# Performance work log

Measured on AMD Instinct MI355X. Metric: run time of the kernel, lower is better.

Reference implementation:

```python
import jax, jax.numpy as jnp
import numpy as np

B, H, W, C, NH = 4, 64, 64, 512, 16
HD = C // NH
BIAS_LEVEL = 0.1
LN_EPS = 1e-5


def layernorm(x, g, b):
    m = jnp.mean(x, axis=-1, keepdims=True)
    v = jnp.mean(jnp.square(x - m), axis=-1, keepdims=True)
    return (x - m) * jax.lax.rsqrt(v + LN_EPS) * g + b


def partition(x, idx):
    # x: [B, L, C] -> windows [nW, S, C]
    xg = x.reshape(B, H, W, C)
    if idx == 0:  # horizontal strips: window = one row of length W
        return xg.reshape(B * H, W, C)
    else:  # vertical strips: window = one column of length H, ordered by column
        return xg.transpose(0, 2, 1, 3).reshape(B * W, H, C)


def unpartition(w, idx):
    # w: [nW, S, C] -> [B, L, C]
    if idx == 0:
        return w.reshape(B, H * W, C)
    else:
        return w.reshape(B, W, H, C).transpose(0, 2, 1, 3).reshape(B, H * W, C)


def eg_attention(q, k, v, res_x, rpe, idx):
    # q,k,v: [B, L, C]; res_x: [B, L, C]; rpe: [1, NH, S, S]
    S = rpe.shape[-1]
    nW = (B * H * W) // S

    def to_heads(t):
        return partition(t, idx).reshape(nW, S, NH, HD).transpose(0, 2, 1, 3)

    qh, kh, vh = to_heads(q), to_heads(k), to_heads(v)  # [nW, NH, S, HD]
    attn = jnp.einsum('whsd,whtd->whst', qh, kh) + BIAS_LEVEL * rpe
    # gating mask from raw scores
    M = jnp.mean(jnp.abs(attn), axis=(1, 2, 3), keepdims=True)  # [nW,1,1,1]
    M = M / jnp.max(M)
    M = jnp.maximum(M, 0.5)
    # L2-normalize rows, trig transform
    norm = jnp.sqrt(jnp.sum(jnp.square(attn), axis=-1, keepdims=True))
    attn = attn / jnp.maximum(norm, 1e-12)
    attn = 1.0 - jnp.cos(attn * (jnp.pi / 2))
    attn = attn * M
    out = jnp.einsum('whst,whtd->whsd', attn, vh)  # [nW, NH, S, HD]
    out = out.transpose(0, 2, 1, 3).reshape(nW, S, C)
    out = unpartition(out, idx)  # [B, L, C]
    # masked residual: res_x is chunked sequentially (row-major), as in the source
    res = res_x.reshape(nW, S, C) * (1.0 - M[:, 0])
    res = res.reshape(B, H * W, C)
    return out + res


def eg_block(x, rpe, idx, ln1_g, ln1_b, wqkv, wproj, bproj, ln2_g, ln2_b,
             wfc1, bfc1, wfc2, bfc2):
    img = layernorm(x, ln1_g, ln1_b)
    qkv = img @ wqkv  # [B, L, 3C]
    q, k, v = jnp.split(qkv, 3, axis=-1)
    att = eg_attention(q, k, v, x, rpe, idx)
    att = att @ wproj + bproj
    x = x + att
    h = layernorm(x, ln2_g, ln2_b)
    h = jax.nn.gelu(h @ wfc1 + bfc1, approximate=False) @ wfc2 + bfc2
    return x + h


def setup_inputs() -> dict:
    key = jax.random.key(0)
    ks = jax.random.split(key, 16)
    d = {
        'x': jax.random.normal(ks[0], (B, H * W, C), jnp.float32),
        'rpe0': jax.random.normal(ks[1], (1, NH, W, W), jnp.float32),
        'rpe1': jax.random.normal(ks[2], (1, NH, H, H), jnp.float32),
    }
    for i, blk in enumerate(['0', '1']):
        kk = jax.random.split(ks[3 + i], 8)
        d['ln1_g' + blk] = jnp.ones((C,), jnp.float32)
        d['ln1_b' + blk] = jnp.zeros((C,), jnp.float32)
        d['wqkv' + blk] = jax.random.normal(kk[0], (C, 3 * C), jnp.float32) * 0.02
        d['wproj' + blk] = jax.random.normal(kk[1], (C, C), jnp.float32) * 0.02
        d['bproj' + blk] = jnp.zeros((C,), jnp.float32)
        d['ln2_g' + blk] = jnp.ones((C,), jnp.float32)
        d['ln2_b' + blk] = jnp.zeros((C,), jnp.float32)
        d['wfc1_' + blk] = jax.random.normal(kk[2], (C, 4 * C), jnp.float32) * 0.02
        d['bfc1_' + blk] = jnp.zeros((4 * C,), jnp.float32)
        d['wfc2_' + blk] = jax.random.normal(kk[3], (4 * C, C), jnp.float32) * 0.02
        d['bfc2_' + blk] = jnp.zeros((C,), jnp.float32)
    return d


def reference(x, rpe0, rpe1,
              ln1_g0, ln1_b0, wqkv0, wproj0, bproj0, ln2_g0, ln2_b0,
              wfc1_0, bfc1_0, wfc2_0, bfc2_0,
              ln1_g1, ln1_b1, wqkv1, wproj1, bproj1, ln2_g1, ln2_b1,
              wfc1_1, bfc1_1, wfc2_1, bfc2_1):
    x = eg_block(x, rpe0, 0, ln1_g0, ln1_b0, wqkv0, wproj0, bproj0,
                 ln2_g0, ln2_b0, wfc1_0, bfc1_0, wfc2_0, bfc2_0)
    x = eg_block(x, rpe1, 1, ln1_g1, ln1_b1, wqkv1, wproj1, bproj1,
                 ln2_g1, ln2_b1, wfc1_1, bfc1_1, wfc2_1, bfc2_1)
    return x
```

## Files before the change

kernel.cpp:

```cpp
#include <hip/hip_runtime.h>
#include <cstdint>
#include <cstddef>

typedef __bf16 bf16;
typedef __attribute__((ext_vector_type(4))) float f32x4;
typedef __attribute__((ext_vector_type(8))) __bf16 bf16x8;
typedef __attribute__((ext_vector_type(4))) __bf16 bf16x4;

static __device__ __forceinline__ f32x4 mfma16(bf16x8 a, bf16x8 b, f32x4 c) {
    return __builtin_amdgcn_mfma_f32_16x16x32_bf16(a, b, c, 0, 0, 0);
}

#define GLOAD_LDS16(gsrc, ldst)                                              \
    __builtin_amdgcn_global_load_lds(                                        \
        (const __attribute__((address_space(1))) void*)(gsrc),               \
        (__attribute__((address_space(3))) void*)(ldst), 16, 0, 0)

__global__ __launch_bounds__(256)
void transpose_cast(const float* __restrict__ W, bf16* __restrict__ Wt, int K, int N) {
    __shared__ float tile[32][33];
    const int n0 = blockIdx.x * 32, k0 = blockIdx.y * 32;
    const int tx = threadIdx.x & 31, ty = threadIdx.x >> 5;
    #pragma unroll
    for (int i = ty; i < 32; i += 8)
        tile[i][tx] = W[(size_t)(k0 + i) * N + n0 + tx];
    __syncthreads();
    #pragma unroll
    for (int i = ty; i < 32; i += 8)
        Wt[(size_t)(n0 + i) * K + k0 + tx] = (bf16)tile[tx][i];
}

__global__ __launch_bounds__(256)
void ln_kernel(const float* __restrict__ x, const float* __restrict__ g,
               const float* __restrict__ b, bf16* __restrict__ out) {
    const int row = blockIdx.x * 4 + (threadIdx.x >> 6);
    const int lane = threadIdx.x & 63;
    const float* p = x + (size_t)row * 512 + lane * 8;
    const float4 a0 = *(const float4*)p;
    const float4 a1 = *(const float4*)(p + 4);
    float vx[8] = {a0.x, a0.y, a0.z, a0.w, a1.x, a1.y, a1.z, a1.w};
    float s = 0.f, ss = 0.f;
    #pragma unroll
    for (int k = 0; k < 8; ++k) { s += vx[k]; ss += vx[k] * vx[k]; }
    #pragma unroll
    for (int m = 1; m < 64; m <<= 1) {
        s  += __shfl_xor(s, m);
        ss += __shfl_xor(ss, m);
    }
    const float mean = s * (1.0f / 512.0f);
    const float var  = ss * (1.0f / 512.0f) - mean * mean;
    const float inv  = rsqrtf(var + 1e-5f);
    const int c0 = lane * 8;
    const float4 g0 = *(const float4*)&g[c0], g1 = *(const float4*)&g[c0 + 4];
    const float4 b0 = *(const float4*)&b[c0], b1 = *(const float4*)&b[c0 + 4];
    const float gv[8] = {g0.x, g0.y, g0.z, g0.w, g1.x, g1.y, g1.z, g1.w};
    const float bv[8] = {b0.x, b0.y, b0.z, b0.w, b1.x, b1.y, b1.z, b1.w};
    bf16x8 o;
    #pragma unroll
    for (int k = 0; k < 8; ++k)
        o[k] = (bf16)((vx[k] - mean) * inv * gv[k] + bv[k]);
    *(bf16x8*)&out[(size_t)row * 512 + c0] = o;
}

template <int EPI>
__global__ __launch_bounds__(256)
void gemm_bt(const bf16* __restrict__ A, const bf16* __restrict__ Bt,
             int N, int K, const float* __restrict__ bias,
             const float* __restrict__ res, float* __restrict__ outf,
             bf16* __restrict__ outh) {
    __shared__ __align__(16) bf16 lsA[128 * 32];
    __shared__ __align__(16) bf16 lsB[128 * 32];
    const int bn = blockIdx.x, bm = blockIdx.y;
    const int tid = threadIdx.x, lane = tid & 63, wv = tid >> 6;
    const int wm = (wv & 1) * 64, wn = (wv >> 1) * 64;
    const int l15 = lane & 15, lg = lane >> 4;
    f32x4 acc[4][4] = {};
    const size_t abase = (size_t)bm * 128 * K;
    const size_t bbase = (size_t)bn * 128 * K;
    const int srow = (lane >> 2);
    const int sseg = (lane & 3) * 8;
    for (int kt = 0; kt < K; kt += 32) {
        __syncthreads();
        #pragma unroll
        for (int c = 0; c < 2; ++c) {
            const int chunk = wv * 2 + c;
            const int row = chunk * 16 + srow;
            GLOAD_LDS16(&A[abase + (size_t)row * K + kt + sseg], &lsA[chunk * 512]);
            GLOAD_LDS16(&Bt[bbase + (size_t)row * K + kt + sseg], &lsB[chunk * 512]);
        }
        __syncthreads();
        bf16x8 af[4], bfr[4];
        #pragma unroll
        for (int i = 0; i < 4; ++i)
            af[i] = *(const bf16x8*)&lsA[(wm + i * 16 + l15) * 32 + lg * 8];
        #pragma unroll
        for (int j = 0; j < 4; ++j)
            bfr[j] = *(const bf16x8*)&lsB[(wn + j * 16 + l15) * 32 + lg * 8];
        #pragma unroll
        for (int i = 0; i < 4; ++i)
            #pragma unroll
            for (int j = 0; j < 4; ++j)
                acc[i][j] = mfma16(af[i], bfr[j], acc[i][j]);
    }
    #pragma unroll
    for (int i = 0; i < 4; ++i) {
        #pragma unroll
        for (int r = 0; r < 4; ++r) {
            const size_t row = (size_t)bm * 128 + wm + i * 16 + lg * 4 + r;
            #pragma unroll
            for (int j = 0; j < 4; ++j) {
                const int col = bn * 128 + wn + j * 16 + l15;
                const float v = acc[i][j][r];
                if constexpr (EPI == 0) {
                    outh[row * N + col] = (bf16)v;
                } else if constexpr (EPI == 1) {
                    outf[row * N + col] = v + bias[col] + res[row * N + col];
                } else {
                    const float t = v + bias[col];
                    const float gl = 0.5f * t * (1.0f + erff(t * 0.70710678118f));
                    outh[row * N + col] = (bf16)gl;
                }
            }
        }
    }
}

__global__ __launch_bounds__(256)
void attn_stats(const bf16* __restrict__ qkv, const float* __restrict__ rpe,
                float* __restrict__ Mraw4, int idx) {
    __shared__ float lsum[4];
    const int bid = blockIdx.x;
    const int w = bid >> 2;
    const int tid = threadIdx.x, lane = tid & 63, wv = tid >> 6;
    const int h = (bid & 3) * 4 + wv;
    const int l15 = lane & 15, lg = lane >> 4;
    const long gbase = (idx == 0) ? (long)w * 64 : ((long)(w >> 6) * 4096 + (w & 63));
    const long gstride = (idx == 0) ? 1 : 64;
    bf16x8 kf[4];
    #pragma unroll
    for (int i = 0; i < 4; ++i) {
        const long gs = gbase + (long)(i * 16 + l15) * gstride;
        kf[i] = *(const bf16x8*)&qkv[gs * 1536 + 512 + h * 32 + lg * 8];
    }
    const float* rh = rpe + h * 4096;
    float asum = 0.f;
    #pragma unroll
    for (int mi = 0; mi < 4; ++mi) {
        const long gs = gbase + (long)(mi * 16 + l15) * gstride;
        const bf16x8 qf = *(const bf16x8*)&qkv[gs * 1536 + h * 32 + lg * 8];
        f32x4 sc[4] = {};
        #pragma unroll
        for (int ni = 0; ni < 4; ++ni) sc[ni] = mfma16(qf, kf[ni], sc[ni]);
        #pragma unroll
        for (int r = 0; r < 4; ++r) {
            const int srow = mi * 16 + lg * 4 + r;
            #pragma unroll
            for (int ni = 0; ni < 4; ++ni)
                asum += fabsf(sc[ni][r] + 0.1f * rh[srow * 64 + ni * 16 + l15]);
        }
    }
    #pragma unroll
    for (int m = 1; m < 64; m <<= 1) asum += __shfl_xor(asum, m);
    if (lane == 0) lsum[wv] = asum;
    __syncthreads();
    if (tid == 0) Mraw4[bid] = lsum[0] + lsum[1] + lsum[2] + lsum[3];
}

__global__ __launch_bounds__(256)
void mcalc(const float* __restrict__ Mraw4, float* __restrict__ Mv) {
    __shared__ float red[4];
    const int t = threadIdx.x, lane = t & 63;
    const float v = (Mraw4[t * 4] + Mraw4[t * 4 + 1] + Mraw4[t * 4 + 2] +
                     Mraw4[t * 4 + 3]) * (1.0f / 65536.0f);
    float m = v;
    #pragma unroll
    for (int msk = 1; msk < 64; msk <<= 1) m = fmaxf(m, __shfl_xor(m, msk));
    if (lane == 0) red[t >> 6] = m;
    __syncthreads();
    const float mm = fmaxf(fmaxf(red[0], red[1]), fmaxf(red[2], red[3]));
    Mv[t] = fmaxf(v / mm, 0.5f);
}

__global__ __launch_bounds__(256)
void attn_apply(const bf16* __restrict__ qkv, const float* __restrict__ rpe,
                const float* __restrict__ Mv, const float* __restrict__ xin,
                bf16* __restrict__ attout, int idx) {
    __shared__ __align__(16) bf16 lsP[4][64 * 64];
    __shared__ __align__(16) bf16 lsVt[4][32 * 64];
    const int bid = blockIdx.x;
    const int w = bid >> 2;
    const int tid = threadIdx.x, lane = tid & 63, wv = tid >> 6;
    const int h = (bid & 3) * 4 + wv;
    const int l15 = lane & 15, lg = lane >> 4;
    const long gbase = (idx == 0) ? (long)w * 64 : ((long)(w >> 6) * 4096 + (w & 63));
    const long gstride = (idx == 0) ? 1 : 64;
    const float Mw = Mv[w];
    bf16* P  = lsP[wv];
    bf16* Vt = lsVt[wv];

    {
        const int d4 = (lane & 7) * 4;
        #pragma unroll
        for (int it = 0; it < 8; ++it) {
            const int t = it * 8 + (lane >> 3);
            const bf16x4 v = *(const bf16x4*)
                &qkv[(gbase + (long)t * gstride) * 1536 + 1024 + h * 32 + d4];
            #pragma unroll
            for (int e = 0; e < 4; ++e) {
                const int d = d4 + e;
                Vt[d * 64 + (t ^ ((d & 7) * 8))] = v[e];
            }
        }
    }
    bf16x8 kf[4];
    #pragma unroll
    for (int i = 0; i < 4; ++i) {
        const long gs = gbase + (long)(i * 16 + l15) * gstride;
        kf[i] = *(const bf16x8*)&qkv[gs * 1536 + 512 + h * 32 + lg * 8];
    }
    const float* rh = rpe + h * 4096;
    #pragma unroll
    for (int mi = 0; mi < 4; ++mi) {
        const long gs = gbase + (long)(mi * 16 + l15) * gstride;
        const bf16x8 qf = *(const bf16x8*)&qkv[gs * 1536 + h * 32 + lg * 8];
        f32x4 sc[4] = {};
        #pragma unroll
        for (int ni = 0; ni < 4; ++ni) sc[ni] = mfma16(qf, kf[ni], sc[ni]);
        #pragma unroll
        for (int r = 0; r < 4; ++r) {
            const int srow = mi * 16 + lg * 4 + r;
            float vv[4], ssq = 0.f;
            #pragma unroll
            for (int ni = 0; ni < 4; ++ni) {
                const float v = sc[ni][r] + 0.1f * rh[srow * 64 + ni * 16 + l15];
                vv[ni] = v;
                ssq += v * v;
            }
            ssq += __shfl_xor(ssq, 1);
            ssq += __shfl_xor(ssq, 2);
            ssq += __shfl_xor(ssq, 4);
            ssq += __shfl_xor(ssq, 8);
            const float is = 1.0f / fmaxf(sqrtf(ssq), 1e-12f);
            #pragma unroll
            for (int ni = 0; ni < 4; ++ni) {
                const float v = (1.0f - __cosf(vv[ni] * is * 1.57079632679f)) * Mw;
                const int col = ni * 16 + l15;
                P[srow * 64 + (col ^ ((srow & 7) * 8))] = (bf16)v;
            }
        }
    }
    f32x4 acc[4][2] = {};
    #pragma unroll
    for (int kk = 0; kk < 2; ++kk) {
        bf16x8 bfr[2];
        #pragma unroll
        for (int dj = 0; dj < 2; ++dj) {
            const int d = dj * 16 + l15;
            bfr[dj] = *(const bf16x8*)&Vt[d * 64 + ((kk * 32 + lg * 8) ^ ((d & 7) * 8))];
        }
        #pragma unroll
        for (int mi = 0; mi < 4; ++mi) {
            const int s = mi * 16 + l15;
            const bf16x8 af = *(const bf16x8*)&P[s * 64 + ((kk * 32 + lg * 8) ^ ((s & 7) * 8))];
            #pragma unroll
            for (int dj = 0; dj < 2; ++dj)
                acc[mi][dj] = mfma16(af, bfr[dj], acc[mi][dj]);
        }
    }
    #pragma unroll
    for (int mi = 0; mi < 4; ++mi) {
        #pragma unroll
        for (int r = 0; r < 4; ++r) {
            const int s = mi * 16 + lg * 4 + r;
            const long gg = gbase + (long)s * gstride;
            const float rm = 1.0f - Mv[(int)(gg >> 6)];
            #pragma unroll
            for (int dj = 0; dj < 2; ++dj) {
                const int d = dj * 16 + l15;
                const size_t oidx = (size_t)gg * 512 + h * 32 + d;
                attout[oidx] = (bf16)(acc[mi][dj][r] + xin[oidx] * rm);
            }
        }
    }
}

extern "C" void kernel_launch(void* const* d_in, const int* in_sizes, int n_in,
                              void* d_out, int out_size, void* d_ws, size_t ws_size,
                              hipStream_t stream) {
    const float* x    = (const float*)d_in[0];
    const float* rpe0 = (const float*)d_in[1];
    const float* rpe1 = (const float*)d_in[2];
    auto W = [&](int i) { return (const float*)d_in[i]; };

    char* ws = (char*)d_ws;
    size_t off = 0;
    auto alloc = [&](size_t bytes) {
        void* p = ws + off;
        off += (bytes + 255) & ~(size_t)255;
        return p;
    };
    bf16 *wqkvT[2], *wprojT[2], *wfc1T[2], *wfc2T[2];
    for (int b = 0; b < 2; ++b) {
        wqkvT[b] = (bf16*)alloc((size_t)1536 * 512 * 2);
        wprojT[b] = (bf16*)alloc((size_t)512 * 512 * 2);
        wfc1T[b] = (bf16*)alloc((size_t)2048 * 512 * 2);
        wfc2T[b] = (bf16*)alloc((size_t)512 * 2048 * 2);
    }
    bf16* IMG = (bf16*)alloc((size_t)16384 * 512 * 2);
    bf16* QKV = (bf16*)alloc((size_t)16384 * 1536 * 2);
    bf16* ATT = (bf16*)alloc((size_t)16384 * 512 * 2);
    bf16* H1  = QKV;
    float* X1    = (float*)alloc((size_t)16384 * 512 * 4);
    float* Mraw4 = (float*)alloc(1024 * 4);
    float* Mv    = (float*)alloc(256 * 4);
    float* XMID  = (float*)d_out;

    auto launchT = [&](const float* Wp, bf16* Wt, int K, int N) {
        transpose_cast<<<dim3(N / 32, K / 32), 256, 0, stream>>>(Wp, Wt, K, N);
    };
    launchT(W(5), wqkvT[0], 512, 1536);
    launchT(W(6), wprojT[0], 512, 512);
    launchT(W(10), wfc1T[0], 512, 2048);
    launchT(W(12), wfc2T[0], 2048, 512);
    launchT(W(16), wqkvT[1], 512, 1536);
    launchT(W(17), wprojT[1], 512, 512);
    launchT(W(21), wfc1T[1], 512, 2048);
    launchT(W(23), wfc2T[1], 2048, 512);

    for (int b = 0; b < 2; ++b) {
        const float* xin = (b == 0) ? x : X1;
        const float* rpe = (b == 0) ? rpe0 : rpe1;
        const int base = (b == 0) ? 3 : 14;
        const float* ln1g = W(base + 0);
        const float* ln1b = W(base + 1);
        const float* bproj = W(base + 4);
        const float* ln2g = W(base + 5);
        const float* ln2b = W(base + 6);
        const float* bfc1 = W(base + 8);
        const float* bfc2 = W(base + 10);

        ln_kernel<<<4096, 256, 0, stream>>>(xin, ln1g, ln1b, IMG);
        gemm_bt<0><<<dim3(12, 128), 256, 0, stream>>>(
            IMG, wqkvT[b], 1536, 512, nullptr, nullptr, nullptr, QKV);
        attn_stats<<<1024, 256, 0, stream>>>(QKV, rpe, Mraw4, b);
        mcalc<<<1, 256, 0, stream>>>(Mraw4, Mv);
        attn_apply<<<1024, 256, 0, stream>>>(QKV, rpe, Mv, xin, ATT, b);
        gemm_bt<1><<<dim3(4, 128), 256, 0, stream>>>(
            ATT, wprojT[b], 512, 512, bproj, xin, XMID, nullptr);
        ln_kernel<<<4096, 256, 0, stream>>>(XMID, ln2g, ln2b, IMG);
        gemm_bt<2><<<dim3(16, 128), 256, 0, stream>>>(
            IMG, wfc1T[b], 2048, 512, bfc1, nullptr, nullptr, H1);
        gemm_bt<1><<<dim3(4, 128), 256, 0, stream>>>(
            H1, wfc2T[b], 512, 2048, bfc2, XMID, (b == 0) ? X1 : XMID, nullptr);
    }
    (void)in_sizes; (void)n_in; (void)out_size; (void)ws_size;
}
```

Measured before the change: 520.1 us.

## Double-buffer GEMM LDS tiles, swizzle LDS layout, and remap workgroups for L2 locality

```diff
diff --git a/kernel.cpp b/kernel.cpp
--- a/kernel.cpp
+++ b/kernel.cpp
@@ -68,40 +68,72 @@
              int N, int K, const float* __restrict__ bias,
              const float* __restrict__ res, float* __restrict__ outf,
              bf16* __restrict__ outh) {
-    __shared__ __align__(16) bf16 lsA[128 * 32];
-    __shared__ __align__(16) bf16 lsB[128 * 32];
-    const int bn = blockIdx.x, bm = blockIdx.y;
+    __shared__ __align__(16) bf16 lsA[2][128 * 32];
+    __shared__ __align__(16) bf16 lsB[2][128 * 32];
+    const int nx = gridDim.x;
+    const int nwg = nx * gridDim.y;
+    const int flat = blockIdx.y * nx + blockIdx.x;
+    const int cpx = nwg >> 3;
+    const int bswz = (flat & 7) * cpx + (flat >> 3);
+    const int bn = bswz % nx, bm = bswz / nx;
+
     const int tid = threadIdx.x, lane = tid & 63, wv = tid >> 6;
     const int wm = (wv & 1) * 64, wn = (wv >> 1) * 64;
     const int l15 = lane & 15, lg = lane >> 4;
-    f32x4 acc[4][4] = {};
     const size_t abase = (size_t)bm * 128 * K;
     const size_t bbase = (size_t)bn * 128 * K;
-    const int srow = (lane >> 2);
-    const int sseg = (lane & 3) * 8;
-    for (int kt = 0; kt < K; kt += 32) {
-        __syncthreads();
-        #pragma unroll
-        for (int c = 0; c < 2; ++c) {
-            const int chunk = wv * 2 + c;
-            const int row = chunk * 16 + srow;
-            GLOAD_LDS16(&A[abase + (size_t)row * K + kt + sseg], &lsA[chunk * 512]);
-            GLOAD_LDS16(&Bt[bbase + (size_t)row * K + kt + sseg], &lsB[chunk * 512]);
-        }
-        __syncthreads();
+    const int srow = lane >> 2;
+    const int slot = lane & 3;
+    const int r0 = (wv * 2 + 0) * 16 + srow;
+    const int r1 = (wv * 2 + 1) * 16 + srow;
+    const int ks0 = (slot ^ ((r0 >> 1) & 3)) * 8;
+    const int ks1 = (slot ^ ((r1 >> 1) & 3)) * 8;
+
+    f32x4 acc[4][4] = {};
+
+    auto stage = [&](int buf, int kt) {
+        GLOAD_LDS16(&A[abase + (size_t)r0 * K + kt + ks0],
+                    &lsA[buf][(wv * 2 + 0) * 512]);
+        GLOAD_LDS16(&A[abase + (size_t)r1 * K + kt + ks1],
+                    &lsA[buf][(wv * 2 + 1) * 512]);
+        GLOAD_LDS16(&Bt[bbase + (size_t)r0 * K + kt + ks0],
+                    &lsB[buf][(wv * 2 + 0) * 512]);
+        GLOAD_LDS16(&Bt[bbase + (size_t)r1 * K + kt + ks1],
+                    &lsB[buf][(wv * 2 + 1) * 512]);
+    };
+    auto compute = [&](int buf) {
         bf16x8 af[4], bfr[4];
         #pragma unroll
-        for (int i = 0; i < 4; ++i)
-            af[i] = *(const bf16x8*)&lsA[(wm + i * 16 + l15) * 32 + lg * 8];
-        #pragma unroll
-        for (int j = 0; j < 4; ++j)
-            bfr[j] = *(const bf16x8*)&lsB[(wn + j * 16 + l15) * 32 + lg * 8];
+        for (int i = 0; i < 4; ++i) {
+            const int r = wm + i * 16 + l15;
+            af[i] = *(const bf16x8*)
+                &lsA[buf][r * 32 + ((lg ^ ((r >> 1) & 3)) * 8)];
+        }
+        #pragma unroll
+        for (int j = 0; j < 4; ++j) {
+            const int r = wn + j * 16 + l15;
+            bfr[j] = *(const bf16x8*)
+                &lsB[buf][r * 32 + ((lg ^ ((r >> 1) & 3)) * 8)];
+        }
         #pragma unroll
         for (int i = 0; i < 4; ++i)
             #pragma unroll
             for (int j = 0; j < 4; ++j)
                 acc[i][j] = mfma16(af[i], bfr[j], acc[i][j]);
-    }
+    };
+
+    const int NK = K >> 5;
+    stage(0, 0);
+    __syncthreads();
+    int cur = 0;
+    for (int t = 0; t < NK - 1; ++t) {
+        stage(cur ^ 1, (t + 1) * 32);
+        compute(cur);
+        __syncthreads();
+        cur ^= 1;
+    }
+    compute(cur);
+
     #pragma unroll
     for (int i = 0; i < 4; ++i) {
         #pragma unroll
```

New measurement: 490.0 us. 5.8% less time.
